# Performance work log

Measured on AMD Instinct MI355X. Metric: run time of the kernel, lower is better.

The kernel has to match this reference:

```python
import jax, jax.numpy as jnp
import numpy as np

B, H, C, D = 32, 12, 512, 768
M = 8            # mentions per entity
EMB, BLK = 768, 8
NCLS, NER = 97, 6
OFFSET = 1       # [CLS] offset as in get_hrt


def setup_inputs() -> dict:
    key = jax.random.key(0)
    ks = jax.random.split(key, 10)
    sequence_output = jax.random.normal(ks[0], (B, C, D), jnp.float32)
    attention = jax.random.uniform(ks[1], (B, H, C, C), jnp.float32)
    ner_tags = jax.random.uniform(ks[2], (B, 2, NER), jnp.float32)
    W_head = jax.random.normal(ks[3], (EMB, 2 * D + NER), jnp.float32) * 0.02
    b_head = jnp.zeros((EMB,), jnp.float32)
    W_tail = jax.random.normal(ks[4], (EMB, 2 * D + NER), jnp.float32) * 0.02
    b_tail = jnp.zeros((EMB,), jnp.float32)
    W_bil = jax.random.normal(ks[5], (NCLS, EMB * BLK), jnp.float32) * 0.02
    b_bil = jnp.zeros((NCLS,), jnp.float32)
    entity_pos = jax.random.randint(ks[6], (B, 2, M), 0, C - 2)
    return {"sequence_output": sequence_output, "attention": attention,
            "ner_tags": ner_tags, "W_head": W_head, "b_head": b_head,
            "W_tail": W_tail, "b_tail": b_tail, "W_bil": W_bil,
            "b_bil": b_bil, "entity_pos": entity_pos}


def reference(sequence_output, attention, ner_tags, W_head, b_head,
              W_tail, b_tail, W_bil, b_bil, entity_pos):
    # --- get_hrt, fully vectorized over batch/entities/mentions ---
    pos = entity_pos + OFFSET                       # [B,2,M], all < C
    bidx = jnp.arange(B)[:, None, None]             # [B,1,1]
    # mention embeddings gather + logsumexp over mentions
    ment_emb = sequence_output[bidx, pos]           # [B,2,M,D]
    ent_emb = jax.scipy.special.logsumexp(ment_emb, axis=2)  # [B,2,D]
    # mention attention-row gather + mean over mentions
    att_t = attention.transpose(0, 2, 1, 3)         # [B,C,H,C]
    ment_att = att_t[bidx, pos]                     # [B,2,M,H,C]
    ent_att = ment_att.mean(axis=2)                 # [B,2,H,C]
    # head/tail = entities 0 and 1
    hs = ent_emb[:, 0]                              # [B,D]
    ht_att = (ent_att[:, 0] * ent_att[:, 1]).mean(axis=1)    # [B,C] (mean over heads)
    ht_att = ht_att / (ht_att.sum(axis=1, keepdims=True) + 1e-5)
    rs = jnp.einsum('bld,bl->bd', sequence_output, ht_att)   # [B,D]
    # --- extractors (note: original code concatenates hs in BOTH inputs) ---
    hs_inp = jnp.concatenate([hs, rs, ner_tags[:, 0]], axis=1)  # [B,2D+NER]
    ts_inp = jnp.concatenate([hs, rs, ner_tags[:, 1]], axis=1)  # faithful to source
    hs_f = jnp.tanh(hs_inp @ W_head.T + b_head)     # [B,EMB]
    ts_f = jnp.tanh(ts_inp @ W_tail.T + b_tail)     # [B,EMB]
    # --- grouped bilinear block ---
    b1 = hs_f.reshape(B, EMB // BLK, BLK)
    b2 = ts_f.reshape(B, EMB // BLK, BLK)
    bl = (b1[:, :, :, None] * b2[:, :, None, :]).reshape(B, EMB * BLK)
    logits = bl @ W_bil.T + b_bil                   # [B,NCLS]
    return logits
```

## Files before the change

kernel.cpp:

```cpp
#include <hip/hip_runtime.h>
#include <math.h>

#define BB 32
#define HH 12
#define CC 512
#define DD 768
#define MM 8
#define NER 6
#define NCLS 97
#define KTOT 1542
#define OFFS 1
#define KCH 193


__global__ void k_att(const float* __restrict__ att, const int* __restrict__ epos,
                      float* __restrict__ raw) {
    int b = blockIdx.x, h = blockIdx.y;
    __shared__ int pos[16];
    if (threadIdx.x < 16) pos[threadIdx.x] = epos[b * 16 + threadIdx.x] + OFFS;
    __syncthreads();
    int c = threadIdx.x;
    const float* base = att + ((size_t)(b * HH + h)) * CC * CC;
    float a0 = 0.f, a1 = 0.f;
#pragma unroll
    for (int m = 0; m < MM; m++) {
        a0 += base[(size_t)pos[m] * CC + c];
        a1 += base[(size_t)pos[MM + m] * CC + c];
    }
    atomicAdd(&raw[b * CC + c], a0 * a1 * (1.0f / (MM * MM * HH)));
}

__global__ void k_rs_part(const float* __restrict__ seq, const float* __restrict__ raw,
                          float* __restrict__ rs_part, float* __restrict__ Sb) {
    int b = blockIdx.x, cc = blockIdx.y, t = threadIdx.x;
    float4 acc = {0.f, 0.f, 0.f, 0.f};
    const float* rw = raw + b * CC + cc * 32;
    const float* sp = seq + ((size_t)b * CC + cc * 32) * DD + t * 4;
    for (int ci = 0; ci < 32; ci++) {
        float w = rw[ci];
        float4 v = *(const float4*)(sp + (size_t)ci * DD);
        acc.x += v.x * w; acc.y += v.y * w; acc.z += v.z * w; acc.w += v.w * w;
    }
    *(float4*)&rs_part[((size_t)(b * 16 + cc)) * DD + t * 4] = acc;
    if (cc == 0) {
        __shared__ float sb[192];
        float s = 0.f;
        for (int c = t; c < CC; c += 192) s += raw[b * CC + c];
        sb[t] = s;
        __syncthreads();
        if (t == 0) {
            float tot = 0.f;
            for (int i = 0; i < 192; i++) tot += sb[i];
            Sb[b] = tot;
        }
    }
}

__global__ void k_rs_hs(const float* __restrict__ seq, const int* __restrict__ epos,
                        const float* __restrict__ rs_part, const float* __restrict__ Sb,
                        float* __restrict__ rs, float* __restrict__ hs) {
    int b = blockIdx.x, t = threadIdx.x;
    __shared__ int pos[MM];
    if (t < MM) pos[t] = epos[b * 16 + t] + OFFS;
    __syncthreads();
    float4 acc = {0.f, 0.f, 0.f, 0.f};
    for (int cc = 0; cc < 16; cc++) {
        float4 p = *(const float4*)&rs_part[((size_t)(b * 16 + cc)) * DD + t * 4];
        acc.x += p.x; acc.y += p.y; acc.z += p.z; acc.w += p.w;
    }
    float inv = 1.0f / (Sb[b] + 1e-5f);
    float4 r = {acc.x * inv, acc.y * inv, acc.z * inv, acc.w * inv};
    *(float4*)&rs[b * DD + t * 4] = r;

    float xs0[MM], xs1[MM], xs2[MM], xs3[MM];
#pragma unroll
    for (int m = 0; m < MM; m++) {
        float4 v = *(const float4*)&seq[((size_t)b * CC + pos[m]) * DD + t * 4];
        xs0[m] = v.x; xs1[m] = v.y; xs2[m] = v.z; xs3[m] = v.w;
    }
    float o[4];
    float* xs[4] = {xs0, xs1, xs2, xs3};
#pragma unroll
    for (int comp = 0; comp < 4; comp++) {
        float mx = xs[comp][0];
#pragma unroll
        for (int m = 1; m < MM; m++) mx = fmaxf(mx, xs[comp][m]);
        float se = 0.f;
#pragma unroll
        for (int m = 0; m < MM; m++) se += expf(xs[comp][m] - mx);
        o[comp] = logf(se) + mx;
    }
    float4 hv = {o[0], o[1], o[2], o[3]};
    *(float4*)&hs[b * DD + t * 4] = hv;
}

__global__ void k_headtail(const float* __restrict__ hs, const float* __restrict__ rs,
                           const float* __restrict__ ner, const float* __restrict__ Wh,
                           const float* __restrict__ Wt, float* __restrict__ accf) {
    int kt = blockIdx.x, jt = blockIdx.y, e = blockIdx.z;
    int kstart = kt * KCH;
    int klen = min(KCH, KTOT - kstart);
    __shared__ float A[32][KCH];
    for (int i = threadIdx.x; i < 32 * KCH; i += 256) {
        int bb = i / KCH, kk = i - bb * KCH;
        int k = kstart + kk;
        float v = 0.f;
        if (k < KTOT) {
            if (k < DD) v = hs[bb * DD + k];
            else if (k < 2 * DD) v = rs[bb * DD + (k - DD)];
            else v = ner[(bb * 2 + e) * NER + (k - 2 * DD)];
        }
        A[bb][kk] = v;
    }
    __syncthreads();
    int b = threadIdx.x & 31, jq = threadIdx.x >> 5;
    int j0 = jt * 64 + jq * 8;
    const float* W = e ? Wt : Wh;
    const float* Wb = W + (size_t)j0 * KTOT + kstart;
    float acc[8] = {0.f, 0.f, 0.f, 0.f, 0.f, 0.f, 0.f, 0.f};
#pragma unroll 4
    for (int kk = 0; kk < klen; kk++) {
        float a = A[b][kk];
#pragma unroll
        for (int jj = 0; jj < 8; jj++) acc[jj] += a * Wb[(size_t)jj * KTOT + kk];
    }
    float* outp = accf + ((size_t)(e * 32 + b)) * DD + j0;
#pragma unroll
    for (int jj = 0; jj < 8; jj++) atomicAdd(&outp[jj], acc[jj]);
}

__global__ void k_tanh(const float* __restrict__ accf, const float* __restrict__ bh,
                       const float* __restrict__ bt, float* __restrict__ fbuf) {
    int x = blockIdx.x * 256 + threadIdx.x;
    int e = x / (BB * DD);
    int r = x - e * (BB * DD);
    int j = r % DD;
    float bias = e ? bt[j] : bh[j];
    fbuf[x] = tanhf(accf[x] + bias);
}

__global__ void k_bil(const float* __restrict__ fbuf, const float* __restrict__ Wb,
                      const float* __restrict__ bbil, float* __restrict__ out) {
    int n = blockIdx.x;
    int g = threadIdx.x & 7, b = threadIdx.x >> 3;
    const float* hsf = fbuf + b * DD;
    const float* tsf = fbuf + (32 + b) * DD;
    const float* W = Wb + (size_t)n * (DD * 8);
    float acc = 0.f;
    for (int t = 0; t < 12; t++) {
        int f = g + 8 * t;
        float4 h0 = *(const float4*)&hsf[f * 8];
        float4 h1 = *(const float4*)&hsf[f * 8 + 4];
        float4 t0 = *(const float4*)&tsf[f * 8];
        float4 t1 = *(const float4*)&tsf[f * 8 + 4];
        float hv[8] = {h0.x, h0.y, h0.z, h0.w, h1.x, h1.y, h1.z, h1.w};
        float tv[8] = {t0.x, t0.y, t0.z, t0.w, t1.x, t1.y, t1.z, t1.w};
        const float* wf = W + f * 64;
#pragma unroll
        for (int i = 0; i < 8; i++) {
            float4 w0 = *(const float4*)&wf[i * 8];
            float4 w1 = *(const float4*)&wf[i * 8 + 4];
            float dot = tv[0] * w0.x + tv[1] * w0.y + tv[2] * w0.z + tv[3] * w0.w
                      + tv[4] * w1.x + tv[5] * w1.y + tv[6] * w1.z + tv[7] * w1.w;
            acc += hv[i] * dot;
        }
    }
    __shared__ float part[32 * 9];
    part[b * 9 + g] = acc;
    __syncthreads();
    if (g == 0) {
        float s = 0.f;
#pragma unroll
        for (int i = 0; i < 8; i++) s += part[b * 9 + i];
        out[b * NCLS + n] = s + bbil[n];
    }
}

extern "C" void kernel_launch(void* const* d_in, const int* in_sizes, int n_in,
                              void* d_out, int out_size, void* d_ws, size_t ws_size,
                              hipStream_t stream) {
    const float* seq  = (const float*)d_in[0];
    const float* att  = (const float*)d_in[1];
    const float* ner  = (const float*)d_in[2];
    const float* Wh   = (const float*)d_in[3];
    const float* bh   = (const float*)d_in[4];
    const float* Wt   = (const float*)d_in[5];
    const float* bt   = (const float*)d_in[6];
    const float* Wbil = (const float*)d_in[7];
    const float* bbil = (const float*)d_in[8];
    const int*   epos = (const int*)d_in[9];
    float* out = (float*)d_out;
    float* ws = (float*)d_ws;

    float* raw     = ws;
    float* Sb      = ws + 16384;
    float* rs_part = ws + 16416;
    float* rs      = ws + 409632;
    float* hs      = ws + 434208;
    float* accf    = ws + 458784;
    float* fbuf    = ws + 507936;

    hipMemsetAsync(raw, 0, (size_t)16384 * 4, stream);
    hipMemsetAsync(accf, 0, (size_t)49152 * 4, stream);

    k_att<<<dim3(BB, HH), 512, 0, stream>>>(att, epos, raw);
    k_rs_part<<<dim3(BB, 16), 192, 0, stream>>>(seq, raw, rs_part, Sb);
    k_rs_hs<<<BB, 192, 0, stream>>>(seq, epos, rs_part, Sb, rs, hs);
    k_headtail<<<dim3(8, 12, 2), 256, 0, stream>>>(hs, rs, ner, Wh, Wt, accf);
    k_tanh<<<192, 256, 0, stream>>>(accf, bh, bt, fbuf);
    k_bil<<<NCLS, 256, 0, stream>>>(fbuf, Wbil, bbil, out);
}
```

Baseline: 567.6 us.

## Fuse logsumexp into attention kernel and restructure head/tail GEMV without atomics

The mention logsumexp moves into an extra y-slice of the attention-gather kernel, and its output goes straight into a packed activation buffer. The rs partial reduction is split into twice as many chunks. The head/tail projection is rewritten so each thread owns one output and loops over all of K in shared-memory chunks, with bias and tanh applied in place. This removes the atomics, the accf memset and the separate tanh kernel, but each block now reloads the full activation matrix eight times and issues fewer, longer-running blocks.

```diff
diff --git a/kernel.cpp b/kernel.cpp
--- a/kernel.cpp
+++ b/kernel.cpp
@@ -6,42 +6,71 @@
 #define CC 512
 #define DD 768
 #define MM 8
-#define NER 6
+#define NERD 6
 #define NCLS 97
 #define KTOT 1542
+#define KMAIN 1536
 #define OFFS 1
-#define KCH 193
-
-
-__global__ void k_att(const float* __restrict__ att, const int* __restrict__ epos,
-                      float* __restrict__ raw) {
+#define KCH 192
+#define APAD 194
+
+
+__global__ void k_att(const float* __restrict__ att, const float* __restrict__ seq,
+                      const int* __restrict__ epos, float* __restrict__ raw,
+                      float* __restrict__ Afull) {
     int b = blockIdx.x, h = blockIdx.y;
     __shared__ int pos[16];
     if (threadIdx.x < 16) pos[threadIdx.x] = epos[b * 16 + threadIdx.x] + OFFS;
     __syncthreads();
-    int c = threadIdx.x;
-    const float* base = att + ((size_t)(b * HH + h)) * CC * CC;
-    float a0 = 0.f, a1 = 0.f;
+    if (h < HH) {
+        int c = threadIdx.x;
+        const float* base = att + ((size_t)(b * HH + h)) * CC * CC;
+        float a0 = 0.f, a1 = 0.f;
+#pragma unroll
+        for (int m = 0; m < MM; m++) {
+            a0 += base[(size_t)pos[m] * CC + c];
+            a1 += base[(size_t)pos[MM + m] * CC + c];
+        }
+        atomicAdd(&raw[b * CC + c], a0 * a1 * (1.0f / (MM * MM * HH)));
+        return;
+    }
+    int t = threadIdx.x;
+    if (t >= 192) return;
+    float xs0[MM], xs1[MM], xs2[MM], xs3[MM];
 #pragma unroll
     for (int m = 0; m < MM; m++) {
-        a0 += base[(size_t)pos[m] * CC + c];
-        a1 += base[(size_t)pos[MM + m] * CC + c];
-    }
-    atomicAdd(&raw[b * CC + c], a0 * a1 * (1.0f / (MM * MM * HH)));
+        float4 v = *(const float4*)&seq[((size_t)b * CC + pos[m]) * DD + t * 4];
+        xs0[m] = v.x; xs1[m] = v.y; xs2[m] = v.z; xs3[m] = v.w;
+    }
+    float o[4];
+    float* xs[4] = {xs0, xs1, xs2, xs3};
+#pragma unroll
+    for (int comp = 0; comp < 4; comp++) {
+        float mx = xs[comp][0];
+#pragma unroll
+        for (int m = 1; m < MM; m++) mx = fmaxf(mx, xs[comp][m]);
+        float se = 0.f;
+#pragma unroll
+        for (int m = 0; m < MM; m++) se += expf(xs[comp][m] - mx);
+        o[comp] = logf(se) + mx;
+    }
+    float4 hv = {o[0], o[1], o[2], o[3]};
+    *(float4*)&Afull[(size_t)b * KMAIN + t * 4] = hv;
 }
 
 __global__ void k_rs_part(const float* __restrict__ seq, const float* __restrict__ raw,
                           float* __restrict__ rs_part, float* __restrict__ Sb) {
     int b = blockIdx.x, cc = blockIdx.y, t = threadIdx.x;
     float4 acc = {0.f, 0.f, 0.f, 0.f};
-    const float* rw = raw + b * CC + cc * 32;
-    const float* sp = seq + ((size_t)b * CC + cc * 32) * DD + t * 4;
-    for (int ci = 0; ci < 32; ci++) {
+    const float* rw = raw + b * CC + cc * 16;
+    const float* sp = seq + ((size_t)b * CC + cc * 16) * DD + t * 4;
+#pragma unroll 4
+    for (int ci = 0; ci < 16; ci++) {
         float w = rw[ci];
         float4 v = *(const float4*)(sp + (size_t)ci * DD);
         acc.x += v.x * w; acc.y += v.y * w; acc.z += v.z * w; acc.w += v.w * w;
     }
-    *(float4*)&rs_part[((size_t)(b * 16 + cc)) * DD + t * 4] = acc;
+    *(float4*)&rs_part[((size_t)(b * 32 + cc)) * DD + t * 4] = acc;
     if (cc == 0) {
         __shared__ float sb[192];
         float s = 0.f;
@@ -56,87 +85,51 @@
     }
 }
 
-__global__ void k_rs_hs(const float* __restrict__ seq, const int* __restrict__ epos,
-                        const float* __restrict__ rs_part, const float* __restrict__ Sb,
-                        float* __restrict__ rs, float* __restrict__ hs) {
+__global__ void k_rs_fin(const float* __restrict__ rs_part, const float* __restrict__ Sb,
+                         float* __restrict__ Afull) {
     int b = blockIdx.x, t = threadIdx.x;
-    __shared__ int pos[MM];
-    if (t < MM) pos[t] = epos[b * 16 + t] + OFFS;
-    __syncthreads();
     float4 acc = {0.f, 0.f, 0.f, 0.f};
-    for (int cc = 0; cc < 16; cc++) {
-        float4 p = *(const float4*)&rs_part[((size_t)(b * 16 + cc)) * DD + t * 4];
+    for (int cc = 0; cc < 32; cc++) {
+        float4 p = *(const float4*)&rs_part[((size_t)(b * 32 + cc)) * DD + t * 4];
         acc.x += p.x; acc.y += p.y; acc.z += p.z; acc.w += p.w;
     }
     float inv = 1.0f / (Sb[b] + 1e-5f);
     float4 r = {acc.x * inv, acc.y * inv, acc.z * inv, acc.w * inv};
-    *(float4*)&rs[b * DD + t * 4] = r;
-
-    float xs0[MM], xs1[MM], xs2[MM], xs3[MM];
-#pragma unroll
-    for (int m = 0; m < MM; m++) {
-        float4 v = *(const float4*)&seq[((size_t)b * CC + pos[m]) * DD + t * 4];
-        xs0[m] = v.x; xs1[m] = v.y; xs2[m] = v.z; xs3[m] = v.w;
-    }
-    float o[4];
-    float* xs[4] = {xs0, xs1, xs2, xs3};
-#pragma unroll
-    for (int comp = 0; comp < 4; comp++) {
-        float mx = xs[comp][0];
-#pragma unroll
-        for (int m = 1; m < MM; m++) mx = fmaxf(mx, xs[comp][m]);
-        float se = 0.f;
-#pragma unroll
-        for (int m = 0; m < MM; m++) se += expf(xs[comp][m] - mx);
-        o[comp] = logf(se) + mx;
-    }
-    float4 hv = {o[0], o[1], o[2], o[3]};
-    *(float4*)&hs[b * DD + t * 4] = hv;
-}
-
-__global__ void k_headtail(const float* __restrict__ hs, const float* __restrict__ rs,
-                           const float* __restrict__ ner, const float* __restrict__ Wh,
-                           const float* __restrict__ Wt, float* __restrict__ accf) {
-    int kt = blockIdx.x, jt = blockIdx.y, e = blockIdx.z;
-    int kstart = kt * KCH;
-    int klen = min(KCH, KTOT - kstart);
-    __shared__ float A[32][KCH];
-    for (int i = threadIdx.x; i < 32 * KCH; i += 256) {
-        int bb = i / KCH, kk = i - bb * KCH;
-        int k = kstart + kk;
-        float v = 0.f;
-        if (k < KTOT) {
-            if (k < DD) v = hs[bb * DD + k];
-            else if (k < 2 * DD) v = rs[bb * DD + (k - DD)];
-            else v = ner[(bb * 2 + e) * NER + (k - 2 * DD)];
-        }
-        A[bb][kk] = v;
-    }
-    __syncthreads();
-    int b = threadIdx.x & 31, jq = threadIdx.x >> 5;
-    int j0 = jt * 64 + jq * 8;
+    *(float4*)&Afull[(size_t)b * KMAIN + DD + t * 4] = r;
+}
+
+__global__ void k_headtail(const float* __restrict__ Afull, const float* __restrict__ ner,
+                           const float* __restrict__ Wh, const float* __restrict__ bh,
+                           const float* __restrict__ Wt, const float* __restrict__ bt,
+                           float* __restrict__ fbuf) {
+    int jt = blockIdx.x, e = blockIdx.y;
+    int tid = threadIdx.x;
+    int b = tid & 31, jq = tid >> 5;
+    int j = jt * 8 + jq;
     const float* W = e ? Wt : Wh;
-    const float* Wb = W + (size_t)j0 * KTOT + kstart;
-    float acc[8] = {0.f, 0.f, 0.f, 0.f, 0.f, 0.f, 0.f, 0.f};
-#pragma unroll 4
-    for (int kk = 0; kk < klen; kk++) {
-        float a = A[b][kk];
-#pragma unroll
-        for (int jj = 0; jj < 8; jj++) acc[jj] += a * Wb[(size_t)jj * KTOT + kk];
-    }
-    float* outp = accf + ((size_t)(e * 32 + b)) * DD + j0;
-#pragma unroll
-    for (int jj = 0; jj < 8; jj++) atomicAdd(&outp[jj], acc[jj]);
-}
-
-__global__ void k_tanh(const float* __restrict__ accf, const float* __restrict__ bh,
-                       const float* __restrict__ bt, float* __restrict__ fbuf) {
-    int x = blockIdx.x * 256 + threadIdx.x;
-    int e = x / (BB * DD);
-    int r = x - e * (BB * DD);
-    int j = r % DD;
-    float bias = e ? bt[j] : bh[j];
-    fbuf[x] = tanhf(accf[x] + bias);
+    const float* bias = e ? bt : bh;
+    __shared__ float A[32][APAD];
+    float acc = 0.f;
+    for (int ch = 0; ch < 8; ch++) {
+        for (int i = tid; i < 32 * KCH; i += 256) {
+            int bb = i / KCH, kk = i - bb * KCH;
+            A[bb][kk] = Afull[(size_t)bb * KMAIN + ch * KCH + kk];
+        }
+        __syncthreads();
+        const float* Wrow = W + (size_t)j * KTOT + ch * KCH;
+#pragma unroll 8
+        for (int kk = 0; kk < KCH; kk += 2) {
+            float2 w = *(const float2*)&Wrow[kk];
+            float2 a = *(const float2*)&A[b][kk];
+            acc += a.x * w.x + a.y * w.y;
+        }
+        __syncthreads();
+    }
+    const float* nr = ner + (b * 2 + e) * NERD;
+    const float* Wn = W + (size_t)j * KTOT + KMAIN;
+#pragma unroll
+    for (int q = 0; q < NERD; q++) acc += nr[q] * Wn[q];
+    fbuf[(size_t)(e * 32 + b) * DD + j] = tanhf(acc + bias[j]);
 }
 
 __global__ void k_bil(const float* __restrict__ fbuf, const float* __restrict__ Wb,
@@ -195,18 +188,14 @@
     float* raw     = ws;
     float* Sb      = ws + 16384;
     float* rs_part = ws + 16416;
-    float* rs      = ws + 409632;
-    float* hs      = ws + 434208;
-    float* accf    = ws + 458784;
-    float* fbuf    = ws + 507936;
+    float* Afull   = ws + 802848;
+    float* fbuf    = ws + 852000;
 
     hipMemsetAsync(raw, 0, (size_t)16384 * 4, stream);
-    hipMemsetAsync(accf, 0, (size_t)49152 * 4, stream);
-
-    k_att<<<dim3(BB, HH), 512, 0, stream>>>(att, epos, raw);
-    k_rs_part<<<dim3(BB, 16), 192, 0, stream>>>(seq, raw, rs_part, Sb);
-    k_rs_hs<<<BB, 192, 0, stream>>>(seq, epos, rs_part, Sb, rs, hs);
-    k_headtail<<<dim3(8, 12, 2), 256, 0, stream>>>(hs, rs, ner, Wh, Wt, accf);
-    k_tanh<<<192, 256, 0, stream>>>(accf, bh, bt, fbuf);
+
+    k_att<<<dim3(BB, HH + 1), 512, 0, stream>>>(att, seq, epos, raw, Afull);
+    k_rs_part<<<dim3(BB, 32), 192, 0, stream>>>(seq, raw, rs_part, Sb);
+    k_rs_fin<<<BB, 192, 0, stream>>>(rs_part, Sb, Afull);
+    k_headtail<<<dim3(96, 2), 256, 0, stream>>>(Afull, ner, Wh, bh, Wt, bt, fbuf);
     k_bil<<<NCLS, 256, 0, stream>>>(fbuf, Wbil, bbil, out);
 }
```

Measured after the change: 580.7 us. 1.02x slower.
